# Performance work log

Hardware: AMD Instinct MI355X
Metric: run time of the kernel (lower is better)

The kernel has to match this reference:

```python
import jax, jax.numpy as jnp
import numpy as np

VOCAB, T, IN, H, L = 32000, 4096, 512, 256, 2


def setup_inputs() -> dict:
    key = jax.random.key(0)
    ks = jax.random.split(key, 32)
    inp = {}
    inp["tokens"] = jax.random.randint(ks[0], (T,), 0, VOCAB)
    inp["emb"] = jax.random.normal(ks[1], (VOCAB, IN), dtype=jnp.float32) * 0.02
    i = 2
    for d in ("f", "b"):
        for l in range(L):
            in_l = IN if l == 0 else H
            inp[f"{d}_Wih{l}"] = jax.random.normal(ks[i], (4 * H, in_l), dtype=jnp.float32) * 0.05; i += 1
            inp[f"{d}_Whh{l}"] = jax.random.normal(ks[i], (4 * H, H), dtype=jnp.float32) * 0.05; i += 1
            inp[f"{d}_bih{l}"] = jnp.zeros((4 * H,), dtype=jnp.float32)
            inp[f"{d}_bhh{l}"] = jnp.zeros((4 * H,), dtype=jnp.float32)
    return inp


def _lstm_layer(x_seq, Wih, Whh, bih, bhh):
    # x_seq: [T, in]; torch.nn.LSTMCell gate order: i, f, g, o
    Hh = Whh.shape[1]
    b = bih + bhh
    def step(carry, x):
        h, c = carry
        g = x @ Wih.T + h @ Whh.T + b           # [4H]
        i_, f_, g_, o_ = jnp.split(g, 4)
        c = jax.nn.sigmoid(f_) * c + jax.nn.sigmoid(i_) * jnp.tanh(g_)
        h = jax.nn.sigmoid(o_) * jnp.tanh(c)
        return (h, c), h
    z = jnp.zeros((Hh,), x_seq.dtype)
    (h, c), hs = jax.lax.scan(step, (z, z), x_seq)
    return hs, h, c                              # [T,H], [H], [H]


def _run_dir(x_seq, params):
    finals = []
    h_seq = x_seq
    for (Wih, Whh, bih, bhh) in params:
        h_seq, h, c = _lstm_layer(h_seq, Wih, Whh, bih, bhh)
        finals.append((c, h))
    return h_seq, finals


def reference(tokens, emb,
              f_Wih0, f_Whh0, f_bih0, f_bhh0, f_Wih1, f_Whh1, f_bih1, f_bhh1,
              b_Wih0, b_Whh0, b_bih0, b_bhh0, b_Wih1, b_Whh1, b_bih1, b_bhh1):
    x = emb[tokens]                              # [T, IN] embedding lookup
    fparams = [(f_Wih0, f_Whh0, f_bih0, f_bhh0), (f_Wih1, f_Whh1, f_bih1, f_bhh1)]
    bparams = [(b_Wih0, b_Whh0, b_bih0, b_bhh0), (b_Wih1, b_Whh1, b_bih1, b_bhh1)]
    f_out, f_fin = _run_dir(x, fparams)          # forward over sequence
    b_out_rev, b_fin = _run_dir(x[::-1], bparams)  # backward over reversed sequence
    b_out = b_out_rev[::-1]
    outputs = jnp.concatenate([f_out, b_out], axis=-1)  # [T, 2H]
    cell_memories = jnp.stack([jnp.stack([f_fin[l][0], b_fin[l][0]]) for l in range(L)])  # [L,2,H]
    hidden_states = jnp.stack([jnp.stack([f_fin[l][1], b_fin[l][1]]) for l in range(L)])  # [L,2,H]
    return cell_memories, hidden_states, outputs
```

## Files before the change

kernel.cpp:

```cpp
#include <hip/hip_runtime.h>
#include <math.h>

#define T_SEQ 4096

__device__ __forceinline__ float sigmoidf_(float x) {
  return 1.0f / (1.0f + expf(-x));
}

__device__ __forceinline__ unsigned long long pack_h(int tag, float h) {
  return ((unsigned long long)(unsigned)tag << 32) |
         (unsigned long long)__float_as_uint(h);
}

__device__ __forceinline__ unsigned long long ld_sc0(const unsigned long long* p) {
  unsigned long long v;
  asm volatile("global_load_dwordx2 %0, %1, off sc0\n\ts_waitcnt vmcnt(0)"
               : "=v"(v) : "v"(p) : "memory");
  return v;
}
__device__ __forceinline__ unsigned long long ld_mall(const unsigned long long* p) {
  unsigned long long v;
  asm volatile("global_load_dwordx2 %0, %1, off sc0 sc1\n\ts_waitcnt vmcnt(0)"
               : "=v"(v) : "v"(p) : "memory");
  return v;
}
__device__ __forceinline__ void st_pub(unsigned long long* p, unsigned long long v) {
  asm volatile("global_store_dwordx2 %0, %1, off sc0\n\t"
               "global_store_dwordx2 %0, %1, off sc0 sc1"
               :: "v"(p), "v"(v) : "memory");
}
__device__ __forceinline__ float poll_h(const unsigned long long* p, unsigned want) {
  int it = 0;
  for (;;) {
    unsigned long long v = ((it & 7) == 7) ? ld_mall(p) : ld_sc0(p);
    if ((unsigned)(v >> 32) == want) return __uint_as_float((unsigned)v);
    ++it;
  }
}

__device__ __forceinline__ void bar() {
  asm volatile("s_waitcnt lgkmcnt(0)" ::: "memory");
  __builtin_amdgcn_s_barrier();
  asm volatile("" ::: "memory");
}

__global__ void gather_emb(const int* __restrict__ tokens,
                           const float4* __restrict__ emb4,
                           float4* __restrict__ X4) {
  int i = blockIdx.x * 256 + threadIdx.x;
  int t = i >> 7;
  int q = i & 127;
  X4[i] = emb4[(long)tokens[t] * 128 + q];
}

__global__ __launch_bounds__(256) void gemm_proj(
    const float* __restrict__ Xf, const float* __restrict__ Xb, int revb,
    const float* __restrict__ Wf, const float* __restrict__ Wb,
    const float* __restrict__ bihf, const float* __restrict__ bhhf,
    const float* __restrict__ bihb, const float* __restrict__ bhhb,
    float* __restrict__ Pf, float* __restrict__ Pb, int K)
{
  const int dirb = blockIdx.z;
  const float* X  = dirb ? Xb : Xf;
  const float* W  = dirb ? Wb : Wf;
  const float* bih = dirb ? bihb : bihf;
  const float* bhh = dirb ? bhhb : bhhf;
  float* Pp = dirb ? Pb : Pf;
  const int rev = dirb ? revb : 0;

  const int bn = blockIdx.x;
  const int bm = blockIdx.y;
  const int tid = threadIdx.x;
  const int tx = tid & 15, ty = tid >> 4;

  __shared__ float Xs[16][68];
  __shared__ float Ws[16][68];

  float acc[4][4] = {{0.f}};

  const int lrow = tid >> 2;
  const int lk4  = (tid & 3) * 4;
  const int xrow = bm * 64 + lrow;
  const int xsrc = rev ? (4095 - xrow) : xrow;
  const float* xptr = X + (long)xsrc * K + lk4;
  const float* wptr = W + (long)(bn * 64 + lrow) * K + lk4;

  for (int k0 = 0; k0 < K; k0 += 16) {
    float4 xv = *(const float4*)(xptr + k0);
    float4 wv = *(const float4*)(wptr + k0);
    __syncthreads();
    Xs[lk4 + 0][lrow] = xv.x; Xs[lk4 + 1][lrow] = xv.y;
    Xs[lk4 + 2][lrow] = xv.z; Xs[lk4 + 3][lrow] = xv.w;
    Ws[lk4 + 0][lrow] = wv.x; Ws[lk4 + 1][lrow] = wv.y;
    Ws[lk4 + 2][lrow] = wv.z; Ws[lk4 + 3][lrow] = wv.w;
    __syncthreads();
    #pragma unroll
    for (int kk = 0; kk < 16; ++kk) {
      float4 a = *(const float4*)(&Xs[kk][ty * 4]);
      float4 b = *(const float4*)(&Ws[kk][tx * 4]);
      acc[0][0] = fmaf(a.x, b.x, acc[0][0]); acc[0][1] = fmaf(a.x, b.y, acc[0][1]);
      acc[0][2] = fmaf(a.x, b.z, acc[0][2]); acc[0][3] = fmaf(a.x, b.w, acc[0][3]);
      acc[1][0] = fmaf(a.y, b.x, acc[1][0]); acc[1][1] = fmaf(a.y, b.y, acc[1][1]);
      acc[1][2] = fmaf(a.y, b.z, acc[1][2]); acc[1][3] = fmaf(a.y, b.w, acc[1][3]);
      acc[2][0] = fmaf(a.z, b.x, acc[2][0]); acc[2][1] = fmaf(a.z, b.y, acc[2][1]);
      acc[2][2] = fmaf(a.z, b.z, acc[2][2]); acc[2][3] = fmaf(a.z, b.w, acc[2][3]);
      acc[3][0] = fmaf(a.w, b.x, acc[3][0]); acc[3][1] = fmaf(a.w, b.y, acc[3][1]);
      acc[3][2] = fmaf(a.w, b.z, acc[3][2]); acc[3][3] = fmaf(a.w, b.w, acc[3][3]);
    }
  }

  const int c0 = bn * 64 + tx * 4;
  #pragma unroll
  for (int i = 0; i < 4; ++i) {
    const int r = bm * 64 + ty * 4 + i;
    float4 o4;
    o4.x = acc[i][0] + bih[c0 + 0] + bhh[c0 + 0];
    o4.y = acc[i][1] + bih[c0 + 1] + bhh[c0 + 1];
    o4.z = acc[i][2] + bih[c0 + 2] + bhh[c0 + 2];
    o4.w = acc[i][3] + bih[c0 + 3] + bhh[c0 + 3];
    *(float4*)(&Pp[(long)r * 1024 + c0]) = o4;
  }
}

__global__ __launch_bounds__(512, 1) void lstm_fused(
    const float* __restrict__ P0f, const float* __restrict__ P0b,
    const float* __restrict__ Whh0f, const float* __restrict__ Whh0b,
    const float* __restrict__ Wih1f, const float* __restrict__ Whh1f,
    const float* __restrict__ bih1f, const float* __restrict__ bhh1f,
    const float* __restrict__ Wih1b, const float* __restrict__ Whh1b,
    const float* __restrict__ bih1b, const float* __restrict__ bhh1b,
    float* __restrict__ out,
    unsigned long long* __restrict__ ring0,
    unsigned long long* __restrict__ h1x)
{
  const int bx = blockIdx.x;
  const int t  = threadIdx.x;

  const int lane8 = bx & 7;
  if (lane8 > 1) return;
  const int d   = lane8;
  const int sub = bx >> 3;

  __shared__ float hx[512];
  __shared__ float part[8 * 264];
  __shared__ float gact[256];
  __shared__ float lds_c[64];

  unsigned long long* ring = ring0 + (long)d * T_SEQ * 256;

  if (sub < 4) {
    const int w = sub;
    const float* __restrict__ P = d ? P0b : P0f;
    const float* __restrict__ W = d ? Whh0b : Whh0f;

    const int kb = t >> 6;
    const int jg = t & 63;

    float wreg[128];
    #pragma unroll
    for (int jj = 0; jj < 4; ++jj) {
      const int m = jg * 4 + jj;
      const int j = (m >> 6) * 256 + w * 64 + (m & 63);
      const float4* wrow = (const float4*)(W + (long)j * 256 + kb * 32);
      #pragma unroll
      for (int kq = 0; kq < 8; ++kq) {
        float4 v = wrow[kq];
        wreg[jj * 32 + kq * 4 + 0] = v.x;
        wreg[jj * 32 + kq * 4 + 1] = v.y;
        wreg[jj * 32 + kq * 4 + 2] = v.z;
        wreg[jj * 32 + kq * 4 + 3] = v.w;
      }
    }

    const long pj   = (long)((t >> 6) * 256 + w * 64 + (t & 63));
    const int ownlo = w * 64;
    const int pcell = (t < ownlo) ? t : t + 64;
    const int fidx  = t - 448;

    float pv_cur = 0.0f;
    if (t < 256) pv_cur = P[pj];
    if (t < 256) hx[t] = 0.0f;
    if (t >= 448) lds_c[fidx] = 0.0f;

    for (int s = 0; s < T_SEQ; ++s) {
      if (s > 0 && t < 192) {
        hx[pcell] = poll_h(ring + (long)(s - 1) * 256 + pcell, (unsigned)s);
      }
      float pv_next = 0.0f;
      if (t < 256 && s + 1 < T_SEQ) pv_next = P[(long)(s + 1) * 1024 + pj];
      bar();

      float a0 = 0.f, a1 = 0.f, a2 = 0.f, a3 = 0.f;
      const float4* h4 = (const float4*)&hx[kb * 32];
      #pragma unroll
      for (int kq = 0; kq < 8; ++kq) {
        float4 hv = h4[kq];
        a0 = fmaf(wreg[0 * 32 + kq * 4 + 0], hv.x, a0);
        a0 = fmaf(wreg[0 * 32 + kq * 4 + 1], hv.y, a0);
        a0 = fmaf(wreg[0 * 32 + kq * 4 + 2], hv.z, a0);
        a0 = fmaf(wreg[0 * 32 + kq * 4 + 3], hv.w, a0);
        a1 = fmaf(wreg[1 * 32 + kq * 4 + 0], hv.x, a1);
        a1 = fmaf(wreg[1 * 32 + kq * 4 + 1], hv.y, a1);
        a1 = fmaf(wreg[1 * 32 + kq * 4 + 2], hv.z, a1);
        a1 = fmaf(wreg[1 * 32 + kq * 4 + 3], hv.w, a1);
        a2 = fmaf(wreg[2 * 32 + kq * 4 + 0], hv.x, a2);
        a2 = fmaf(wreg[2 * 32 + kq * 4 + 1], hv.y, a2);
        a2 = fmaf(wreg[2 * 32 + kq * 4 + 2], hv.z, a2);
        a2 = fmaf(wreg[2 * 32 + kq * 4 + 3], hv.w, a2);
        a3 = fmaf(wreg[3 * 32 + kq * 4 + 0], hv.x, a3);
        a3 = fmaf(wreg[3 * 32 + kq * 4 + 1], hv.y, a3);
        a3 = fmaf(wreg[3 * 32 + kq * 4 + 2], hv.z, a3);
        a3 = fmaf(wreg[3 * 32 + kq * 4 + 3], hv.w, a3);
      }
      float4 av; av.x = a0; av.y = a1; av.z = a2; av.w = a3;
      *(float4*)(&part[kb * 264 + jg * 4]) = av;
      bar();

      if (t < 256) {
        float g = pv_cur;
        #pragma unroll
        for (int q = 0; q < 8; ++q) g += part[q * 264 + t];
        gact[t] = ((t >> 6) == 2) ? tanhf(g) : sigmoidf_(g);
        pv_cur = pv_next;
      }
      bar();

      if (t >= 448) {
        const int cell = ownlo + fidx;
        float c = gact[64 + fidx] * lds_c[fidx] + gact[fidx] * gact[128 + fidx];
        float h = gact[192 + fidx] * tanhf(c);
        lds_c[fidx] = c;
        hx[cell] = h;
        st_pub(ring + (long)s * 256 + cell, pack_h(s + 1, h));
        if (s == T_SEQ - 1) {
          out[d * 256 + cell] = c;
          out[1024 + d * 256 + cell] = h;
        }
      }
    }
  } else {
    const int w1 = sub - 4;
    const float* __restrict__ Wih = d ? Wih1b : Wih1f;
    const float* __restrict__ Whh = d ? Whh1b : Whh1f;
    const float* __restrict__ bih = d ? bih1b : bih1f;
    const float* __restrict__ bhh = d ? bhh1b : bhh1f;
    unsigned long long* slot = h1x + d * 512;
    float* hout = d ? (out + 2048 + (long)4095 * 512 + 256) : (out + 2048);
    const long hstr = d ? -512 : 512;

    const int kb = t >> 6;
    const int jg = t & 63;

    float wreg[2][64];
    #pragma unroll
    for (int rr = 0; rr < 2; ++rr) {
      const int m = jg * 2 + rr;
      const int j = (m >> 5) * 256 + w1 * 32 + (m & 31);
      const float* srcw = (kb < 4) ? (Wih + (long)j * 256 + kb * 64)
                                   : (Whh + (long)j * 256 + (kb - 4) * 64);
      const float4* s4 = (const float4*)srcw;
      #pragma unroll
      for (int q = 0; q < 16; ++q) {
        float4 v = s4[q];
        wreg[rr][q * 4 + 0] = v.x; wreg[rr][q * 4 + 1] = v.y;
        wreg[rr][q * 4 + 2] = v.z; wreg[rr][q * 4 + 3] = v.w;
      }
    }

    const int fidx = t - 480;
    const int t2   = t - 256;
    const int pc1  = (t2 < w1 * 32) ? t2 : t2 + 32;

    float bsum = 0.0f;
    if (t < 128) {
      const int j = (t >> 5) * 256 + w1 * 32 + (t & 31);
      bsum = bih[j] + bhh[j];
    }

    if (t >= 480) {
      lds_c[fidx] = 0.0f;
      hx[256 + w1 * 32 + fidx] = 0.0f;
    }

    for (int s = 0; s < T_SEQ; ++s) {
      if (t < 256) {
        hx[t] = poll_h(ring + (long)s * 256 + t, (unsigned)(s + 1));
      } else if (t < 480) {
        hx[256 + pc1] = poll_h(slot + ((s + 1) & 1) * 256 + pc1, (unsigned)s);
      }
      bar();

      float a0 = 0.f, a1 = 0.f;
      const float4* h4 = (const float4*)&hx[kb * 64];
      #pragma unroll
      for (int q = 0; q < 16; ++q) {
        float4 hv = h4[q];
        a0 = fmaf(wreg[0][q * 4 + 0], hv.x, a0);
        a0 = fmaf(wreg[0][q * 4 + 1], hv.y, a0);
        a0 = fmaf(wreg[0][q * 4 + 2], hv.z, a0);
        a0 = fmaf(wreg[0][q * 4 + 3], hv.w, a0);
        a1 = fmaf(wreg[1][q * 4 + 0], hv.x, a1);
        a1 = fmaf(wreg[1][q * 4 + 1], hv.y, a1);
        a1 = fmaf(wreg[1][q * 4 + 2], hv.z, a1);
        a1 = fmaf(wreg[1][q * 4 + 3], hv.w, a1);
      }
      float2 av2; av2.x = a0; av2.y = a1;
      *(float2*)(&part[kb * 264 + jg * 2]) = av2;
      bar();

      if (t < 128) {
        float g = bsum;
        #pragma unroll
        for (int q = 0; q < 8; ++q) g += part[q * 264 + t];
        gact[t] = ((t >> 5) == 2) ? tanhf(g) : sigmoidf_(g);
      }
      bar();

      if (t >= 480) {
        const int cell = w1 * 32 + fidx;
        float c = gact[32 + fidx] * lds_c[fidx] + gact[fidx] * gact[64 + fidx];
        float h = gact[96 + fidx] * tanhf(c);
        lds_c[fidx] = c;
        hx[256 + cell] = h;
        st_pub(&slot[(s & 1) * 256 + cell], pack_h(s + 1, h));
        hout[(long)s * hstr + cell] = h;
        if (s == T_SEQ - 1) {
          out[512 + d * 256 + cell] = c;
          out[1024 + 512 + d * 256 + cell] = h;
        }
      }
    }
  }
}

extern "C" void kernel_launch(void* const* d_in, const int* in_sizes, int n_in,
                              void* d_out, int out_size, void* d_ws, size_t ws_size,
                              hipStream_t stream) {
  const int*   tokens = (const int*)d_in[0];
  const float* emb    = (const float*)d_in[1];
  const float* fWih0 = (const float*)d_in[2];
  const float* fWhh0 = (const float*)d_in[3];
  const float* fbih0 = (const float*)d_in[4];
  const float* fbhh0 = (const float*)d_in[5];
  const float* fWih1 = (const float*)d_in[6];
  const float* fWhh1 = (const float*)d_in[7];
  const float* fbih1 = (const float*)d_in[8];
  const float* fbhh1 = (const float*)d_in[9];
  const float* bWih0 = (const float*)d_in[10];
  const float* bWhh0 = (const float*)d_in[11];
  const float* bbih0 = (const float*)d_in[12];
  const float* bbhh0 = (const float*)d_in[13];
  const float* bWih1 = (const float*)d_in[14];
  const float* bWhh1 = (const float*)d_in[15];
  const float* bbih1 = (const float*)d_in[16];
  const float* bbhh1 = (const float*)d_in[17];

  float* out = (float*)d_out;
  float* ws  = (float*)d_ws;

  float* X   = ws;
  float* P0f = ws + 4194304;
  float* P0b = ws + 8388608;
  unsigned long long* ring0 = (unsigned long long*)ws;
  unsigned long long* h1x   = (unsigned long long*)(ws + 12582912);

  gather_emb<<<2048, 256, 0, stream>>>(tokens, (const float4*)emb, (float4*)X);

  gemm_proj<<<dim3(16, 64, 2), 256, 0, stream>>>(
      X, X, 1, fWih0, bWih0, fbih0, fbhh0, bbih0, bbhh0, P0f, P0b, 512);

  hipMemsetAsync(ring0, 0, (size_t)2 * T_SEQ * 256 * sizeof(unsigned long long), stream);
  hipMemsetAsync(h1x, 0, 1024 * sizeof(unsigned long long), stream);

  lstm_fused<<<dim3(96), 512, 0, stream>>>(
      P0f, P0b, fWhh0, bWhh0,
      fWih1, fWhh1, fbih1, fbhh1,
      bWih1, bWhh1, bbih1, bbhh1,
      out, ring0, h1x);
}
```

Measured before the change: 7.902 ms.

## Claim XCD-local workgroups dynamically and fuse cell update into gate threads

Workgroups now read their hardware XCC id and atomically claim roles, so each direction's twelve workgroups land on the same XCD and cross-block h exchange stays within one die. The grid grows to 768 and extra blocks exit early. Gate rows are interleaved i,f,g,o per four lanes, so the cell update runs with wave shuffles instead of a separate LDS pass, removing one barrier per timestep. The change also reassigns polling threads, keeps weights in named float4 registers, and uses the slower MALL-level poll less often. The claim protocol adds startup atomics and relies on the XCC id register and on all claimed blocks being co-resident.

Result: slower. 11.88 ms (+50.4%).

```diff
diff --git a/kernel.cpp b/kernel.cpp
--- a/kernel.cpp
+++ b/kernel.cpp
@@ -32,7 +32,7 @@
 __device__ __forceinline__ float poll_h(const unsigned long long* p, unsigned want) {
   int it = 0;
   for (;;) {
-    unsigned long long v = ((it & 7) == 7) ? ld_mall(p) : ld_sc0(p);
+    unsigned long long v = ((it & 15) == 15) ? ld_mall(p) : ld_sc0(p);
     if ((unsigned)(v >> 32) == want) return __uint_as_float((unsigned)v);
     ++it;
   }
@@ -43,6 +43,14 @@
   __builtin_amdgcn_s_barrier();
   asm volatile("" ::: "memory");
 }
+
+#define DECL_W8(p) float4 p##0, p##1, p##2, p##3, p##4, p##5, p##6, p##7
+#define LOAD_W8(p, src) do { const float4* _s = (const float4*)(src); \
+  p##0=_s[0]; p##1=_s[1]; p##2=_s[2]; p##3=_s[3]; \
+  p##4=_s[4]; p##5=_s[5]; p##6=_s[6]; p##7=_s[7]; } while (0)
+#define FMA4(acc, W_, H_) do { acc = fmaf((W_).x, (H_).x, acc); \
+  acc = fmaf((W_).y, (H_).y, acc); acc = fmaf((W_).z, (H_).z, acc); \
+  acc = fmaf((W_).w, (H_).w, acc); } while (0)
 
 __global__ void gather_emb(const int* __restrict__ tokens,
                            const float4* __restrict__ emb4,
@@ -131,59 +139,62 @@
     const float* __restrict__ bih1b, const float* __restrict__ bhh1b,
     float* __restrict__ out,
     unsigned long long* __restrict__ ring0,
-    unsigned long long* __restrict__ h1x)
+    unsigned long long* __restrict__ h1x,
+    int* __restrict__ claim)
 {
-  const int bx = blockIdx.x;
-  const int t  = threadIdx.x;
-
-  const int lane8 = bx & 7;
-  if (lane8 > 1) return;
-  const int d   = lane8;
-  const int sub = bx >> 3;
-
+  const int t = threadIdx.x;
+
+  __shared__ int s_dir, s_sub;
   __shared__ float hx[512];
   __shared__ float part[8 * 264];
-  __shared__ float gact[256];
-  __shared__ float lds_c[64];
+
+  int hwv;
+  asm volatile("s_getreg_b32 %0, hwreg(HW_REG_XCC_ID)" : "=s"(hwv));
+  const int myxcd = hwv & 7;
+  if (t == 0) {
+    int* cnt  = claim;
+    int* xdir = claim + 16;
+    int r = atomicAdd(&cnt[myxcd], 1);
+    if (r == 0) {
+      int dslot = atomicAdd(&cnt[8], 1);
+      atomicExch(&xdir[myxcd], (dslot < 2) ? (dslot + 1) : 3);
+    }
+    int dv;
+    do { dv = atomicAdd(&xdir[myxcd], 0); } while (dv == 0);
+    s_dir = (dv <= 2 && r < 12) ? (dv - 1) : -1;
+    s_sub = r;
+  }
+  __syncthreads();
+  if (s_dir < 0) return;
+  const int d   = s_dir;
+  const int sub = s_sub;
 
   unsigned long long* ring = ring0 + (long)d * T_SEQ * 256;
 
   if (sub < 4) {
     const int w = sub;
+    const int wbase = w * 64;
     const float* __restrict__ P = d ? P0b : P0f;
     const float* __restrict__ W = d ? Whh0b : Whh0f;
 
     const int kb = t >> 6;
     const int jg = t & 63;
 
-    float wreg[128];
-    #pragma unroll
-    for (int jj = 0; jj < 4; ++jj) {
-      const int m = jg * 4 + jj;
-      const int j = (m >> 6) * 256 + w * 64 + (m & 63);
-      const float4* wrow = (const float4*)(W + (long)j * 256 + kb * 32);
-      #pragma unroll
-      for (int kq = 0; kq < 8; ++kq) {
-        float4 v = wrow[kq];
-        wreg[jj * 32 + kq * 4 + 0] = v.x;
-        wreg[jj * 32 + kq * 4 + 1] = v.y;
-        wreg[jj * 32 + kq * 4 + 2] = v.z;
-        wreg[jj * 32 + kq * 4 + 3] = v.w;
-      }
-    }
-
-    const long pj   = (long)((t >> 6) * 256 + w * 64 + (t & 63));
-    const int ownlo = w * 64;
-    const int pcell = (t < ownlo) ? t : t + 64;
-    const int fidx  = t - 448;
-
-    float pv_cur = 0.0f;
-    if (t < 256) pv_cur = P[pj];
-    if (t < 256) hx[t] = 0.0f;
-    if (t >= 448) lds_c[fidx] = 0.0f;
+    DECL_W8(wa); DECL_W8(wb); DECL_W8(wc); DECL_W8(wd);
+    LOAD_W8(wa, W + (long)(0 * 256 + wbase + jg) * 256 + kb * 32);
+    LOAD_W8(wb, W + (long)(1 * 256 + wbase + jg) * 256 + kb * 32);
+    LOAD_W8(wc, W + (long)(2 * 256 + wbase + jg) * 256 + kb * 32);
+    LOAD_W8(wd, W + (long)(3 * 256 + wbase + jg) * 256 + kb * 32);
+
+    const long pj = (long)((t & 3) * 256 + wbase + (t >> 2));
+
+    float pv_cur = 0.0f, c_prev = 0.0f;
+    if (t < 256) { pv_cur = P[pj]; hx[t] = 0.0f; }
 
     for (int s = 0; s < T_SEQ; ++s) {
-      if (s > 0 && t < 192) {
+      if (s > 0 && t >= 256 && t < 448) {
+        const int q = t - 256;
+        const int pcell = (q < wbase) ? q : q + 64;
         hx[pcell] = poll_h(ring + (long)(s - 1) * 256 + pcell, (unsigned)s);
       }
       float pv_next = 0.0f;
@@ -192,26 +203,11 @@
 
       float a0 = 0.f, a1 = 0.f, a2 = 0.f, a3 = 0.f;
       const float4* h4 = (const float4*)&hx[kb * 32];
-      #pragma unroll
-      for (int kq = 0; kq < 8; ++kq) {
-        float4 hv = h4[kq];
-        a0 = fmaf(wreg[0 * 32 + kq * 4 + 0], hv.x, a0);
-        a0 = fmaf(wreg[0 * 32 + kq * 4 + 1], hv.y, a0);
-        a0 = fmaf(wreg[0 * 32 + kq * 4 + 2], hv.z, a0);
-        a0 = fmaf(wreg[0 * 32 + kq * 4 + 3], hv.w, a0);
-        a1 = fmaf(wreg[1 * 32 + kq * 4 + 0], hv.x, a1);
-        a1 = fmaf(wreg[1 * 32 + kq * 4 + 1], hv.y, a1);
-        a1 = fmaf(wreg[1 * 32 + kq * 4 + 2], hv.z, a1);
-        a1 = fmaf(wreg[1 * 32 + kq * 4 + 3], hv.w, a1);
-        a2 = fmaf(wreg[2 * 32 + kq * 4 + 0], hv.x, a2);
-        a2 = fmaf(wreg[2 * 32 + kq * 4 + 1], hv.y, a2);
-        a2 = fmaf(wreg[2 * 32 + kq * 4 + 2], hv.z, a2);
-        a2 = fmaf(wreg[2 * 32 + kq * 4 + 3], hv.w, a2);
-        a3 = fmaf(wreg[3 * 32 + kq * 4 + 0], hv.x, a3);
-        a3 = fmaf(wreg[3 * 32 + kq * 4 + 1], hv.y, a3);
-        a3 = fmaf(wreg[3 * 32 + kq * 4 + 2], hv.z, a3);
-        a3 = fmaf(wreg[3 * 32 + kq * 4 + 3], hv.w, a3);
-      }
+      #define L0STEP(q) do { float4 hv = h4[q]; FMA4(a0, wa##q, hv); \
+        FMA4(a1, wb##q, hv); FMA4(a2, wc##q, hv); FMA4(a3, wd##q, hv); } while (0)
+      L0STEP(0); L0STEP(1); L0STEP(2); L0STEP(3);
+      L0STEP(4); L0STEP(5); L0STEP(6); L0STEP(7);
+      #undef L0STEP
       float4 av; av.x = a0; av.y = a1; av.z = a2; av.w = a3;
       *(float4*)(&part[kb * 264 + jg * 4]) = av;
       bar();
@@ -220,26 +216,33 @@
         float g = pv_cur;
         #pragma unroll
         for (int q = 0; q < 8; ++q) g += part[q * 264 + t];
-        gact[t] = ((t >> 6) == 2) ? tanhf(g) : sigmoidf_(g);
+        float act = ((t & 3) == 2) ? tanhf(g) : sigmoidf_(g);
+        float y  = __shfl_xor(act, 1);
+        float zx = __shfl_xor(act, 2);
+        float zy = __shfl_xor(y, 2);
+        const bool l1b = (t & 1), h1b = (t & 2);
+        float i_ = h1b ? (l1b ? zy : zx) : (l1b ? y : act);
+        float f_ = h1b ? (l1b ? zx : zy) : (l1b ? act : y);
+        float g_ = h1b ? (l1b ? y : act) : (l1b ? zy : zx);
+        float o_ = h1b ? (l1b ? act : y) : (l1b ? zx : zy);
+        float c = f_ * c_prev + i_ * g_;
+        c_prev = c;
+        float h = o_ * tanhf(c);
+        if ((t & 3) == 0) {
+          const int gc = wbase + (t >> 2);
+          hx[gc] = h;
+          st_pub(ring + (long)s * 256 + gc, pack_h(s + 1, h));
+          if (s == T_SEQ - 1) {
+            out[d * 256 + gc] = c;
+            out[1024 + d * 256 + gc] = h;
+          }
+        }
         pv_cur = pv_next;
       }
-      bar();
-
-      if (t >= 448) {
-        const int cell = ownlo + fidx;
-        float c = gact[64 + fidx] * lds_c[fidx] + gact[fidx] * gact[128 + fidx];
-        float h = gact[192 + fidx] * tanhf(c);
-        lds_c[fidx] = c;
-        hx[cell] = h;
-        st_pub(ring + (long)s * 256 + cell, pack_h(s + 1, h));
-        if (s == T_SEQ - 1) {
-          out[d * 256 + cell] = c;
-          out[1024 + d * 256 + cell] = h;
-        }
-      }
     }
   } else {
     const int w1 = sub - 4;
+    const int wbase1 = w1 * 32;
     const float* __restrict__ Wih = d ? Wih1b : Wih1f;
     const float* __restrict__ Whh = d ? Whh1b : Whh1f;
     const float* __restrict__ bih = d ? bih1b : bih1f;
@@ -251,59 +254,51 @@
     const int kb = t >> 6;
     const int jg = t & 63;
 
-    float wreg[2][64];
-    #pragma unroll
-    for (int rr = 0; rr < 2; ++rr) {
-      const int m = jg * 2 + rr;
-      const int j = (m >> 5) * 256 + w1 * 32 + (m & 31);
-      const float* srcw = (kb < 4) ? (Wih + (long)j * 256 + kb * 64)
-                                   : (Whh + (long)j * 256 + (kb - 4) * 64);
-      const float4* s4 = (const float4*)srcw;
-      #pragma unroll
-      for (int q = 0; q < 16; ++q) {
-        float4 v = s4[q];
-        wreg[rr][q * 4 + 0] = v.x; wreg[rr][q * 4 + 1] = v.y;
-        wreg[rr][q * 4 + 2] = v.z; wreg[rr][q * 4 + 3] = v.w;
-      }
-    }
-
-    const int fidx = t - 480;
-    const int t2   = t - 256;
-    const int pc1  = (t2 < w1 * 32) ? t2 : t2 + 32;
-
-    float bsum = 0.0f;
+    const int m0 = jg * 2, m1 = m0 + 1;
+    const int j0 = (m0 & 3) * 256 + wbase1 + (m0 >> 2);
+    const int j1 = (m1 & 3) * 256 + wbase1 + (m1 >> 2);
+    const float* s0 = (kb < 4) ? (Wih + (long)j0 * 256 + kb * 64)
+                               : (Whh + (long)j0 * 256 + (kb - 4) * 64);
+    const float* s1 = (kb < 4) ? (Wih + (long)j1 * 256 + kb * 64)
+                               : (Whh + (long)j1 * 256 + (kb - 4) * 64);
+    DECL_W8(ua); DECL_W8(ub); DECL_W8(uc); DECL_W8(ud);
+    LOAD_W8(ua, s0); LOAD_W8(ub, s0 + 32);
+    LOAD_W8(uc, s1); LOAD_W8(ud, s1 + 32);
+
+    float bsum = 0.0f, c_prev = 0.0f;
     if (t < 128) {
-      const int j = (t >> 5) * 256 + w1 * 32 + (t & 31);
+      const int j = (t & 3) * 256 + wbase1 + (t >> 2);
       bsum = bih[j] + bhh[j];
-    }
-
-    if (t >= 480) {
-      lds_c[fidx] = 0.0f;
-      hx[256 + w1 * 32 + fidx] = 0.0f;
+      if ((t & 3) == 0) hx[256 + wbase1 + (t >> 2)] = 0.0f;
     }
 
     for (int s = 0; s < T_SEQ; ++s) {
-      if (t < 256) {
-        hx[t] = poll_h(ring + (long)s * 256 + t, (unsigned)(s + 1));
-      } else if (t < 480) {
-        hx[256 + pc1] = poll_h(slot + ((s + 1) & 1) * 256 + pc1, (unsigned)s);
+      if (t >= 128 && t < 384) {
+        const int c0_ = t - 128;
+        hx[c0_] = poll_h(ring + (long)s * 256 + c0_, (unsigned)(s + 1));
+      } else {
+        int q1 = -1;
+        if (t < 128) { if ((t & 3) != 0) q1 = (t >> 2) * 3 + (t & 3) - 1; }
+        else q1 = 96 + (t - 384);
+        if (q1 >= 0) {
+          const int pc1 = (q1 < wbase1) ? q1 : q1 + 32;
+          hx[256 + pc1] = poll_h(slot + ((s + 1) & 1) * 256 + pc1, (unsigned)s);
+        }
       }
       bar();
 
       float a0 = 0.f, a1 = 0.f;
       const float4* h4 = (const float4*)&hx[kb * 64];
-      #pragma unroll
-      for (int q = 0; q < 16; ++q) {
-        float4 hv = h4[q];
-        a0 = fmaf(wreg[0][q * 4 + 0], hv.x, a0);
-        a0 = fmaf(wreg[0][q * 4 + 1], hv.y, a0);
-        a0 = fmaf(wreg[0][q * 4 + 2], hv.z, a0);
-        a0 = fmaf(wreg[0][q * 4 + 3], hv.w, a0);
-        a1 = fmaf(wreg[1][q * 4 + 0], hv.x, a1);
-        a1 = fmaf(wreg[1][q * 4 + 1], hv.y, a1);
-        a1 = fmaf(wreg[1][q * 4 + 2], hv.z, a1);
-        a1 = fmaf(wreg[1][q * 4 + 3], hv.w, a1);
-      }
+      #define L1STEPA(q) do { float4 hv = h4[q];     FMA4(a0, ua##q, hv); \
+        FMA4(a1, uc##q, hv); } while (0)
+      #define L1STEPB(q) do { float4 hv = h4[8 + q]; FMA4(a0, ub##q, hv); \
+        FMA4(a1, ud##q, hv); } while (0)
+      L1STEPA(0); L1STEPA(1); L1STEPA(2); L1STEPA(3);
+      L1STEPA(4); L1STEPA(5); L1STEPA(6); L1STEPA(7);
+      L1STEPB(0); L1STEPB(1); L1STEPB(2); L1STEPB(3);
+      L1STEPB(4); L1STEPB(5); L1STEPB(6); L1STEPB(7);
+      #undef L1STEPA
+      #undef L1STEPB
       float2 av2; av2.x = a0; av2.y = a1;
       *(float2*)(&part[kb * 264 + jg * 2]) = av2;
       bar();
@@ -312,21 +307,27 @@
         float g = bsum;
         #pragma unroll
         for (int q = 0; q < 8; ++q) g += part[q * 264 + t];
-        gact[t] = ((t >> 5) == 2) ? tanhf(g) : sigmoidf_(g);
-      }
-      bar();
-
-      if (t >= 480) {
-        const int cell = w1 * 32 + fidx;
-        float c = gact[32 + fidx] * lds_c[fidx] + gact[fidx] * gact[64 + fidx];
-        float h = gact[96 + fidx] * tanhf(c);
-        lds_c[fidx] = c;
-        hx[256 + cell] = h;
-        st_pub(&slot[(s & 1) * 256 + cell], pack_h(s + 1, h));
-        hout[(long)s * hstr + cell] = h;
-        if (s == T_SEQ - 1) {
-          out[512 + d * 256 + cell] = c;
-          out[1024 + 512 + d * 256 + cell] = h;
+        float act = ((t & 3) == 2) ? tanhf(g) : sigmoidf_(g);
+        float y  = __shfl_xor(act, 1);
+        float zx = __shfl_xor(act, 2);
+        float zy = __shfl_xor(y, 2);
+        const bool l1b = (t & 1), h1b = (t & 2);
+        float i_ = h1b ? (l1b ? zy : zx) : (l1b ? y : act);
+        float f_ = h1b ? (l1b ? zx : zy) : (l1b ? act : y);
+        float g_ = h1b ? (l1b ? y : act) : (l1b ? zy : zx);
+        float o_ = h1b ? (l1b ? act : y) : (l1b ? zx : zy);
+        float c = f_ * c_prev + i_ * g_;
+        c_prev = c;
+        float h = o_ * tanhf(c);
+        if ((t & 3) == 0) {
+          const int gc = wbase1 + (t >> 2);
+          hx[256 + gc] = h;
+          st_pub(&slot[(s & 1) * 256 + gc], pack_h(s + 1, h));
+          hout[(long)s * hstr + gc] = h;
+          if (s == T_SEQ - 1) {
+            out[512 + d * 256 + gc] = c;
+            out[1024 + 512 + d * 256 + gc] = h;
+          }
         }
       }
     }
@@ -363,6 +364,7 @@
   float* P0b = ws + 8388608;
   unsigned long long* ring0 = (unsigned long long*)ws;
   unsigned long long* h1x   = (unsigned long long*)(ws + 12582912);
+  int* claim = (int*)(ws + 12584960);
 
   gather_emb<<<2048, 256, 0, stream>>>(tokens, (const float4*)emb, (float4*)X);
 
@@ -371,10 +373,11 @@
 
   hipMemsetAsync(ring0, 0, (size_t)2 * T_SEQ * 256 * sizeof(unsigned long long), stream);
   hipMemsetAsync(h1x, 0, 1024 * sizeof(unsigned long long), stream);
-
-  lstm_fused<<<dim3(96), 512, 0, stream>>>(
+  hipMemsetAsync(claim, 0, 32 * sizeof(int), stream);
+
+  lstm_fused<<<dim3(768), 512, 0, stream>>>(
       P0f, P0b, fWhh0, bWhh0,
       fWih1, fWhh1, fbih1, fbhh1,
       bWih1, bWhh1, bbih1, bbhh1,
-      out, ring0, h1x);
-}
+      out, ring0, h1x, claim);
+}
```
